# Performance work log

Hardware: AMD Instinct MI355X
Metric: run time of the kernel (lower is better)

## Reference

```python
import jax, jax.numpy as jnp
import numpy as np

HEADS = 8
DIM_HEAD = 64
SCALE = DIM_HEAD ** -0.5


def setup_inputs() -> dict:
    key = jax.random.key(0)
    ks = jax.random.split(key, 7)
    B, N, Dq = 2, 4096, 512
    M, Dc = 4096, 768
    inner = HEADS * DIM_HEAD  # 512
    x = jax.random.normal(ks[0], (B, N, Dq), dtype=jnp.float32)
    context = jax.random.normal(ks[1], (B, M, Dc), dtype=jnp.float32)
    # weights stored [in, out] (torch Linear weight transposed)
    Wq = jax.random.normal(ks[2], (Dq, inner), dtype=jnp.float32) * (Dq ** -0.5)
    Wk = jax.random.normal(ks[3], (Dc, inner), dtype=jnp.float32) * (Dc ** -0.5)
    Wv = jax.random.normal(ks[4], (Dc, inner), dtype=jnp.float32) * (Dc ** -0.5)
    Wo = jax.random.normal(ks[5], (inner, Dq), dtype=jnp.float32) * (inner ** -0.5)
    bo = jax.random.normal(ks[6], (Dq,), dtype=jnp.float32) * 0.01
    return {"x": x, "context": context, "Wq": Wq, "Wk": Wk, "Wv": Wv, "Wo": Wo, "bo": bo}


def reference(x, context, Wq, Wk, Wv, Wo, bo):
    B, N, _ = x.shape
    M = context.shape[1]
    h, d = HEADS, DIM_HEAD
    q = (x @ Wq).reshape(B, N, h, d)                      # b n h d
    k = ((context @ Wk) * SCALE).reshape(B, M, h, d)      # scale applied to k, as in source
    v = (context @ Wv).reshape(B, M, h, d)
    scores = jnp.einsum('bnhd,bmhd->bhnm', q, k)          # full QK^T
    attn = jax.nn.softmax(scores, axis=-1)
    out = jnp.einsum('bhnm,bmhd->bnhd', attn, v).reshape(B, N, h * d)
    return out @ Wo + bo  # dropout p=0.0 -> identity
```

## Files before the change

### kernel.cpp

```cpp
#include <hip/hip_runtime.h>

typedef unsigned short u16;
typedef __attribute__((ext_vector_type(4))) unsigned short u16x4;
typedef __attribute__((ext_vector_type(8))) unsigned short u16x8;
typedef __attribute__((ext_vector_type(8))) short s16x8;
typedef __attribute__((ext_vector_type(4))) float f32x4;
typedef __attribute__((ext_vector_type(16))) float f32x16;
typedef __attribute__((ext_vector_type(4))) unsigned int u32x4;

#define LOG2E 1.4426950408889634f

__device__ __forceinline__ u16 f2bf(float f) {
    return __builtin_bit_cast(unsigned short, static_cast<__bf16>(f));
}

__device__ __forceinline__ float bf2f(u16 v) {
    return __builtin_bit_cast(float, (unsigned)v << 16);
}

__device__ __forceinline__ float fexp2(float x) {
#if __has_builtin(__builtin_amdgcn_exp2f)
    return __builtin_amdgcn_exp2f(x);
#else
    return exp2f(x);
#endif
}

__device__ __forceinline__ s16x8 ld_frag(const u16* p) {
    return __builtin_bit_cast(s16x8, *reinterpret_cast<const u16x8*>(p));
}

__device__ __forceinline__ f32x4 mfma16(s16x8 a, s16x8 b, f32x4 c) {
    return __builtin_amdgcn_mfma_f32_16x16x32_bf16(a, b, c, 0, 0, 0);
}

__device__ __forceinline__ f32x16 mfma32(s16x8 a, s16x8 b, f32x16 c) {
    return __builtin_amdgcn_mfma_f32_32x32x16_bf16(a, b, c, 0, 0, 0);
}

__device__ __forceinline__ unsigned cvt_pk_bf16(float lo, float hi2) {
    unsigned r;
    asm("v_cvt_pk_bf16_f32 %0, %1, %2" : "=v"(r) : "v"(lo), "v"(hi2));
    return r;
}

__device__ __forceinline__ void plane32_swap(unsigned& x, unsigned& y) {
#if __has_builtin(__builtin_amdgcn_permlane32_swap)
    auto r = __builtin_amdgcn_permlane32_swap(x, y, false, false);
    x = r[0];
    y = r[1];
#else
    asm("v_permlane32_swap_b32 %0, %1" : "+v"(x), "+v"(y));
#endif
}

__device__ __forceinline__ void async16(const u16* g, u16* lds) {
    __builtin_amdgcn_global_load_lds(
        (__attribute__((address_space(1))) void*)const_cast<u16*>(g),
        (__attribute__((address_space(3))) void*)lds, 16, 0, 0);
}

__global__ __launch_bounds__(256) void cvt_fused_kernel(const float* __restrict__ x,
                                                        const float* __restrict__ ctx,
                                                        u16* __restrict__ xb,
                                                        u16* __restrict__ cb) {
    int i = blockIdx.x * 256 + threadIdx.x;
    const float* in;
    u16* out;
    int idx;
    if (i < 524288) {
        in = x; out = xb; idx = i;
    } else {
        in = ctx; out = cb; idx = i - 524288;
    }
    const f32x4* p = (const f32x4*)in + ((size_t)idx << 1);
    f32x4 a = p[0], c = p[1];
    u16x8 v;
    v[0] = f2bf(a[0]); v[1] = f2bf(a[1]); v[2] = f2bf(a[2]); v[3] = f2bf(a[3]);
    v[4] = f2bf(c[0]); v[5] = f2bf(c[1]); v[6] = f2bf(c[2]); v[7] = f2bf(c[3]);
    *((u16x8*)out + idx) = v;
}

__global__ __launch_bounds__(256) void wtrans4_kernel(
    const float* __restrict__ Wq, const float* __restrict__ Wk, const float* __restrict__ Wv,
    const float* __restrict__ Wo, u16* __restrict__ Wqt, u16* __restrict__ Wkt,
    u16* __restrict__ Wvt, u16* __restrict__ Wot) {
    __shared__ float t[32][33];
    const float* W;
    u16* Wt;
    int Kd;
    float scale;
    switch (blockIdx.z) {
        case 0: W = Wq; Wt = Wqt; Kd = 512; scale = 1.0f; break;
        case 1: W = Wk; Wt = Wkt; Kd = 768; scale = 0.125f * LOG2E; break;
        case 2: W = Wv; Wt = Wvt; Kd = 768; scale = 1.0f; break;
        default: W = Wo; Wt = Wot; Kd = 512; scale = 1.0f; break;
    }
    const int k0 = blockIdx.x << 5, n0 = blockIdx.y << 5;
    if (k0 >= Kd) return;
    const int tx = threadIdx.x, ty = threadIdx.y;
#pragma unroll
    for (int i = 0; i < 32; i += 8)
        t[ty + i][tx] = W[(size_t)(k0 + ty + i) * 512 + n0 + tx] * scale;
    __syncthreads();
#pragma unroll
    for (int i = 0; i < 32; i += 8)
        Wt[(size_t)(n0 + ty + i) * Kd + k0 + tx] = f2bf(t[tx][ty + i]);
}

template <int MODE>
__device__ __forceinline__ void gemm_body(u16* __restrict__ Ab, u16* __restrict__ Bb,
                                          const u16* __restrict__ A, const u16* __restrict__ Bt,
                                          void* __restrict__ Cv, const float* __restrict__ bias,
                                          int K) {
    const int tid = threadIdx.x;
    const int w = tid >> 6, l = tid & 63;
    const int lg = l >> 4, lq = l & 15;
    const int wm = w >> 1, wn = w & 1;
    const int bm = blockIdx.y, bn = blockIdx.x;
    const int KT = K >> 6;

    f32x4 acc[4][4];
#pragma unroll
    for (int i = 0; i < 4; i++)
#pragma unroll
        for (int j = 0; j < 4; j++) acc[i][j] = (f32x4){0.f, 0.f, 0.f, 0.f};

    const u16* Ag0 = A + (size_t)bm * 128 * K;
    const u16* Bg0 = Bt + (size_t)bn * 128 * K;
    const int srow = l >> 3, scol = (l & 7) << 3;

    auto stage = [&](int kt, int buf) {
#pragma unroll
        for (int i = 0; i < 4; i++) {
            const int c = (w << 2) + i;
            const int row = (c << 3) + srow;
            async16(Ag0 + (size_t)row * K + kt * 64 + scol, Ab + (buf << 13) + (c << 9));
            async16(Bg0 + (size_t)row * K + kt * 64 + scol, Bb + (buf << 13) + (c << 9));
        }
    };

    stage(0, 0);
    for (int kt = 0; kt < KT; ++kt) {
        __syncthreads();
        if (kt + 1 < KT) stage(kt + 1, (kt + 1) & 1);
        const u16* As = Ab + ((kt & 1) << 13);
        const u16* Bs = Bb + ((kt & 1) << 13);
#pragma unroll
        for (int s = 0; s < 2; s++) {
            s16x8 af[4], bfr[4];
#pragma unroll
            for (int mt = 0; mt < 4; mt++)
                af[mt] = ld_frag(As + ((wm << 6) + (mt << 4) + lq) * 64 + (s << 5) + (lg << 3));
#pragma unroll
            for (int nt = 0; nt < 4; nt++)
                bfr[nt] = ld_frag(Bs + ((wn << 6) + (nt << 4) + lq) * 64 + (s << 5) + (lg << 3));
#pragma unroll
            for (int mt = 0; mt < 4; mt++)
#pragma unroll
                for (int nt = 0; nt < 4; nt++)
                    acc[mt][nt] = mfma16(af[mt], bfr[nt], acc[mt][nt]);
        }
    }
    const int row0 = bm * 128 + (wm << 6);
    const int col0 = bn * 128 + (wn << 6);
    if constexpr (MODE == 0) {
        u16* C = (u16*)Cv;
#pragma unroll
        for (int mt = 0; mt < 4; mt++)
#pragma unroll
            for (int nt = 0; nt < 4; nt++)
#pragma unroll
                for (int r = 0; r < 4; r++)
                    C[(size_t)(row0 + (mt << 4) + (lg << 2) + r) * 512 + col0 + (nt << 4) + lq] =
                        f2bf(acc[mt][nt][r]);
    } else if constexpr (MODE == 3) {
        float* C = (float*)Cv;
        float bv[4];
#pragma unroll
        for (int nt = 0; nt < 4; nt++) bv[nt] = bias[col0 + (nt << 4) + lq];
#pragma unroll
        for (int mt = 0; mt < 4; mt++)
#pragma unroll
            for (int nt = 0; nt < 4; nt++)
#pragma unroll
                for (int r = 0; r < 4; r++)
                    C[(size_t)(row0 + (mt << 4) + (lg << 2) + r) * 512 + col0 + (nt << 4) + lq] =
                        acc[mt][nt][r] + bv[nt];
    } else {
        u16* C = (u16*)Cv;
#pragma unroll
        for (int mt = 0; mt < 4; mt++)
#pragma unroll
            for (int nt = 0; nt < 4; nt++)
#pragma unroll
                for (int r = 0; r < 4; r++) {
                    const int m = row0 + (mt << 4) + (lg << 2) + r;
                    const int feat = col0 + (nt << 4) + lq;
                    const int bh = ((m >> 12) << 3) + (feat >> 6);
                    const int d = feat & 63;
                    const int kv = m & 4095;
                    const int T = kv >> 5, kvl = kv & 31;
                    size_t off;
                    if constexpr (MODE == 1) {
                        const int lane = kvl + (((d >> 3) & 1) << 5);
                        off = ((size_t)(((bh << 7) + T) << 2) + (d >> 4)) * 512 + (lane << 3) +
                              (d & 7);
                    } else {
                        const int lane = (d & 31) + (((kvl >> 3) & 1) << 5);
                        const int fi = ((kvl >> 4) << 1) + (d >> 5);
                        off = ((size_t)(((bh << 7) + T) << 2) + fi) * 512 + (lane << 3) +
                              (kvl & 7);
                    }
                    C[off] = f2bf(acc[mt][nt][r]);
                }
    }
}

__global__ __launch_bounds__(256, 2) void proj_gemm_kernel(
    const u16* __restrict__ xb, const u16* __restrict__ cb, const u16* __restrict__ Wqt,
    const u16* __restrict__ Wkt, const u16* __restrict__ Wvt, u16* __restrict__ Qb,
    u16* __restrict__ Kp, u16* __restrict__ Vp) {
    __shared__ u16 Ab[2][8192];
    __shared__ u16 Bb[2][8192];
    const int z = blockIdx.z;
    if (z == 0)
        gemm_body<0>(&Ab[0][0], &Bb[0][0], xb, Wqt, Qb, nullptr, 512);
    else if (z == 1)
        gemm_body<1>(&Ab[0][0], &Bb[0][0], cb, Wkt, Kp, nullptr, 768);
    else
        gemm_body<2>(&Ab[0][0], &Bb[0][0], cb, Wvt, Vp, nullptr, 768);
}

__global__ __launch_bounds__(256, 2) void out_gemm_kernel(const u16* __restrict__ Ob,
                                                          const u16* __restrict__ Wot,
                                                          float* __restrict__ out,
                                                          const float* __restrict__ bias) {
    __shared__ u16 Ab[2][8192];
    __shared__ u16 Bb[2][8192];
    gemm_body<3>(&Ab[0][0], &Bb[0][0], Ob, Wot, out, bias, 512);
}

__global__ __launch_bounds__(256, 3) void attn_kernel(const u16* __restrict__ Qb,
                                                      const u16* __restrict__ Kp,
                                                      const u16* __restrict__ Vp,
                                                      u16* __restrict__ Opart,
                                                      float* __restrict__ Lpart) {
    __shared__ u16 Kl[2][2048];
    __shared__ u16 Vl[2][2048];
    const int tid = threadIdx.x;
    const int w = tid >> 6, l = tid & 63;
    const int lq = l & 31, hi = l >> 5;
    const int bid = blockIdx.x;
    const int swz = ((bid & 7) << 8) + (bid >> 3);
    const int bh = swz >> 7, qtg = (swz >> 2) & 31, kvseg = swz & 3;
    const int qt = (qtg << 2) + w;
    const int wid = (((bh << 7) + qt) << 2) + kvseg;
    const int b = bh >> 3, h = bh & 7;

    const u16* Qp = Qb + (size_t)(b * 4096 + (qt << 5) + lq) * 512 + (h << 6) + (hi << 3);
    s16x8 qf[4];
#pragma unroll
    for (int s = 0; s < 4; s++) qf[s] = ld_frag(Qp + (s << 4));

    const u16* Kg = Kp + ((size_t)(bh << 7) + (kvseg << 5)) * 2048;
    const u16* Vg = Vp + ((size_t)(bh << 7) + (kvseg << 5)) * 2048;
    const int gsrc = (w << 9) + (l << 3);
    const int ldst = w << 9;
    const int roff = l << 3;

    f32x16 oacc0 = {}, oacc1 = {};
    float rs = 0.f;

    async16(Kg + gsrc, &Kl[0][ldst]);
    async16(Vg + gsrc, &Vl[0][ldst]);

    for (int t = 0; t < 32; ++t) {
        const int buf = t & 1;
        __syncthreads();
        if (t + 1 < 32) {
            async16(Kg + (size_t)(t + 1) * 2048 + gsrc, &Kl[buf ^ 1][ldst]);
            async16(Vg + (size_t)(t + 1) * 2048 + gsrc, &Vl[buf ^ 1][ldst]);
        }
        const u16* Kb_ = Kl[buf];
        const u16* Vb_ = Vl[buf];

        s16x8 kf[4];
#pragma unroll
        for (int s = 0; s < 4; s++) kf[s] = ld_frag(Kb_ + (s << 9) + roff);
        f32x16 sacc = {};
        __builtin_amdgcn_s_setprio(1);
#pragma unroll
        for (int s = 0; s < 4; s++) sacc = mfma32(kf[s], qf[s], sacc);
        __builtin_amdgcn_s_setprio(0);

#pragma unroll
        for (int r = 0; r < 16; r++) sacc[r] = fexp2(sacc[r]);
        {
            float t0 = (sacc[0] + sacc[1]) + (sacc[2] + sacc[3]);
            float t1 = (sacc[4] + sacc[5]) + (sacc[6] + sacc[7]);
            float t2 = (sacc[8] + sacc[9]) + (sacc[10] + sacc[11]);
            float t3 = (sacc[12] + sacc[13]) + (sacc[14] + sacc[15]);
            rs += (t0 + t1) + (t2 + t3);
        }

        s16x8 aw[2];
#pragma unroll
        for (int sp = 0; sp < 2; sp++) {
            const int base2 = sp << 3;
            unsigned X1 = cvt_pk_bf16(sacc[base2 + 0], sacc[base2 + 1]);
            unsigned Y1 = cvt_pk_bf16(sacc[base2 + 4], sacc[base2 + 5]);
            unsigned X2 = cvt_pk_bf16(sacc[base2 + 2], sacc[base2 + 3]);
            unsigned Y2 = cvt_pk_bf16(sacc[base2 + 6], sacc[base2 + 7]);
            plane32_swap(X1, Y1);
            plane32_swap(X2, Y2);
            u32x4 wv;
            wv[0] = X1; wv[1] = X2; wv[2] = Y1; wv[3] = Y2;
            aw[sp] = __builtin_bit_cast(s16x8, wv);
        }

        s16x8 vf[4];
#pragma unroll
        for (int f = 0; f < 4; f++) vf[f] = ld_frag(Vb_ + (f << 9) + roff);
        __builtin_amdgcn_s_setprio(1);
#pragma unroll
        for (int sp = 0; sp < 2; sp++) {
            oacc0 = mfma32(aw[sp], vf[(sp << 1) + 0], oacc0);
            oacc1 = mfma32(aw[sp], vf[(sp << 1) + 1], oacc1);
        }
        __builtin_amdgcn_s_setprio(0);
    }

    u16* Ow = Opart + ((size_t)wid << 11);
#pragma unroll
    for (int r = 0; r < 16; r++) Ow[(r << 6) + l] = f2bf(oacc0[r]);
#pragma unroll
    for (int r = 0; r < 16; r++) Ow[((16 + r) << 6) + l] = f2bf(oacc1[r]);
    rs += __shfl_xor(rs, 32);
    if (l < 32) Lpart[(wid << 5) + l] = rs;
}

__global__ __launch_bounds__(256) void merge_kernel(const u16* __restrict__ Op,
                                                    const float* __restrict__ Lp,
                                                    u16* __restrict__ Ob) {
    const int g = blockIdx.x * 256 + threadIdx.x;
    const int slot = g >> 9;
    const int idx4 = (g & 511) << 2;
    const int dtr = idx4 >> 6;
    const int r = dtr & 15, dt = dtr >> 4;
    const int lane0 = idx4 & 63;
    const int q = (r & 3) + ((r >> 2) << 3) + ((lane0 >> 5) << 2);
    float lsum = 0.f;
#pragma unroll
    for (int p = 0; p < 4; p++) lsum += Lp[(slot << 7) + (p << 5) + q];
    const float ri = 1.f / lsum;
    float acc[4] = {0.f, 0.f, 0.f, 0.f};
#pragma unroll
    for (int p = 0; p < 4; p++) {
        const u16x4 a = *(const u16x4*)(Op + ((size_t)slot << 13) + (p << 11) + idx4);
#pragma unroll
        for (int j = 0; j < 4; j++) acc[j] += bf2f(a[j]);
    }
    u16x4 o;
#pragma unroll
    for (int j = 0; j < 4; j++) o[j] = f2bf(acc[j] * ri);
    const int bh = slot >> 7, qt = slot & 127;
    const int row = ((bh >> 3) << 12) + (qt << 5) + q;
    const int d = (lane0 & 31) + (dt << 5);
    *(u16x4*)(Ob + (size_t)row * 512 + ((bh & 7) << 6) + d) = o;
}

extern "C" void kernel_launch(void* const* d_in, const int* in_sizes, int n_in, void* d_out,
                              int out_size, void* d_ws, size_t ws_size, hipStream_t stream) {
    const float* x = (const float*)d_in[0];
    const float* ctx = (const float*)d_in[1];
    const float* Wq = (const float*)d_in[2];
    const float* Wk = (const float*)d_in[3];
    const float* Wv = (const float*)d_in[4];
    const float* Wo = (const float*)d_in[5];
    const float* bo = (const float*)d_in[6];
    float* out = (float*)d_out;

    char* ws = (char*)d_ws;
    u16* xb  = (u16*)(ws);
    u16* cb  = (u16*)(ws + 8388608);
    u16* Opart   = (u16*)(ws);
    float* Lpart = (float*)(ws + 33554432);
    u16* Qb  = (u16*)(ws + 34603008);
    u16* Ob  = (u16*)(ws + 34603008);
    u16* Kp  = (u16*)(ws + 42991616);
    u16* Vp  = (u16*)(ws + 51380224);
    u16* Wqt = (u16*)(ws + 59768832);
    u16* Wkt = (u16*)(ws + 60293120);
    u16* Wvt = (u16*)(ws + 61079552);
    u16* Wot = (u16*)(ws + 61865984);

    cvt_fused_kernel<<<dim3(5120), dim3(256), 0, stream>>>(x, ctx, xb, cb);
    wtrans4_kernel<<<dim3(24, 16, 4), dim3(32, 8), 0, stream>>>(Wq, Wk, Wv, Wo, Wqt, Wkt, Wvt,
                                                                Wot);
    proj_gemm_kernel<<<dim3(4, 64, 3), dim3(256), 0, stream>>>(xb, cb, Wqt, Wkt, Wvt, Qb, Kp, Vp);
    attn_kernel<<<dim3(2048), dim3(256), 0, stream>>>(Qb, Kp, Vp, Opart, Lpart);
    merge_kernel<<<dim3(4096), dim3(256), 0, stream>>>(Opart, Lpart, Ob);
    out_gemm_kernel<<<dim3(4, 64), dim3(256), 0, stream>>>(Ob, Wot, out, bo);
}
```

Measured before the change: 156.2 us.

## Fuse prep kernels, double attention KV tile per stage, widen merge vectors

Merges the fp32-to-bf16 conversion and weight transpose into a single prep launch, which removes one kernel launch. The attention loop now stages two 32-key sub-tiles per barrier (16 iterations instead of 32), halving sync count at the cost of double the LDS per block. The merge kernel handles 8 bf16 elements per thread with 128-bit loads and stores, halving its grid. The larger LDS footprint may reduce attention occupancy.

```diff
diff --git a/kernel.cpp b/kernel.cpp
--- a/kernel.cpp
+++ b/kernel.cpp
@@ -60,52 +60,56 @@
         (__attribute__((address_space(3))) void*)lds, 16, 0, 0);
 }
 
-__global__ __launch_bounds__(256) void cvt_fused_kernel(const float* __restrict__ x,
-                                                        const float* __restrict__ ctx,
-                                                        u16* __restrict__ xb,
-                                                        u16* __restrict__ cb) {
-    int i = blockIdx.x * 256 + threadIdx.x;
-    const float* in;
-    u16* out;
-    int idx;
-    if (i < 524288) {
-        in = x; out = xb; idx = i;
-    } else {
-        in = ctx; out = cb; idx = i - 524288;
-    }
-    const f32x4* p = (const f32x4*)in + ((size_t)idx << 1);
-    f32x4 a = p[0], c = p[1];
-    u16x8 v;
-    v[0] = f2bf(a[0]); v[1] = f2bf(a[1]); v[2] = f2bf(a[2]); v[3] = f2bf(a[3]);
-    v[4] = f2bf(c[0]); v[5] = f2bf(c[1]); v[6] = f2bf(c[2]); v[7] = f2bf(c[3]);
-    *((u16x8*)out + idx) = v;
-}
-
-__global__ __launch_bounds__(256) void wtrans4_kernel(
-    const float* __restrict__ Wq, const float* __restrict__ Wk, const float* __restrict__ Wv,
-    const float* __restrict__ Wo, u16* __restrict__ Wqt, u16* __restrict__ Wkt,
+__global__ __launch_bounds__(256) void prep_kernel(
+    const float* __restrict__ x, const float* __restrict__ ctx, const float* __restrict__ Wq,
+    const float* __restrict__ Wk, const float* __restrict__ Wv, const float* __restrict__ Wo,
+    u16* __restrict__ xb, u16* __restrict__ cb, u16* __restrict__ Wqt, u16* __restrict__ Wkt,
     u16* __restrict__ Wvt, u16* __restrict__ Wot) {
     __shared__ float t[32][33];
-    const float* W;
-    u16* Wt;
-    int Kd;
-    float scale;
-    switch (blockIdx.z) {
-        case 0: W = Wq; Wt = Wqt; Kd = 512; scale = 1.0f; break;
-        case 1: W = Wk; Wt = Wkt; Kd = 768; scale = 0.125f * LOG2E; break;
-        case 2: W = Wv; Wt = Wvt; Kd = 768; scale = 1.0f; break;
-        default: W = Wo; Wt = Wot; Kd = 512; scale = 1.0f; break;
+    const int bidx = blockIdx.x;
+    const int tid = threadIdx.x;
+    if (bidx < 5120) {
+        int i = bidx * 256 + tid;
+        const float* in;
+        u16* out;
+        int idx;
+        if (i < 524288) {
+            in = x; out = xb; idx = i;
+        } else {
+            in = ctx; out = cb; idx = i - 524288;
+        }
+        const f32x4* p = (const f32x4*)in + ((size_t)idx << 1);
+        f32x4 a = p[0], c = p[1];
+        u16x8 v;
+        v[0] = f2bf(a[0]); v[1] = f2bf(a[1]); v[2] = f2bf(a[2]); v[3] = f2bf(a[3]);
+        v[4] = f2bf(c[0]); v[5] = f2bf(c[1]); v[6] = f2bf(c[2]); v[7] = f2bf(c[3]);
+        *((u16x8*)out + idx) = v;
+    } else {
+        const int zb = bidx - 5120;
+        const int z = zb / 384;
+        const int rem = zb - z * 384;
+        const int kx = rem % 24, ny = rem / 24;
+        const float* W;
+        u16* Wt;
+        int Kd;
+        float scale;
+        switch (z) {
+            case 0: W = Wq; Wt = Wqt; Kd = 512; scale = 1.0f; break;
+            case 1: W = Wk; Wt = Wkt; Kd = 768; scale = 0.125f * LOG2E; break;
+            case 2: W = Wv; Wt = Wvt; Kd = 768; scale = 1.0f; break;
+            default: W = Wo; Wt = Wot; Kd = 512; scale = 1.0f; break;
+        }
+        const int k0 = kx << 5, n0 = ny << 5;
+        if (k0 >= Kd) return;
+        const int tx = tid & 31, ty = tid >> 5;
+#pragma unroll
+        for (int i = 0; i < 32; i += 8)
+            t[ty + i][tx] = W[(size_t)(k0 + ty + i) * 512 + n0 + tx] * scale;
+        __syncthreads();
+#pragma unroll
+        for (int i = 0; i < 32; i += 8)
+            Wt[(size_t)(n0 + ty + i) * Kd + k0 + tx] = f2bf(t[tx][ty + i]);
     }
-    const int k0 = blockIdx.x << 5, n0 = blockIdx.y << 5;
-    if (k0 >= Kd) return;
-    const int tx = threadIdx.x, ty = threadIdx.y;
-#pragma unroll
-    for (int i = 0; i < 32; i += 8)
-        t[ty + i][tx] = W[(size_t)(k0 + ty + i) * 512 + n0 + tx] * scale;
-    __syncthreads();
-#pragma unroll
-    for (int i = 0; i < 32; i += 8)
-        Wt[(size_t)(n0 + ty + i) * Kd + k0 + tx] = f2bf(t[tx][ty + i]);
 }
 
 template <int MODE>
@@ -246,8 +250,8 @@
                                                       const u16* __restrict__ Vp,
                                                       u16* __restrict__ Opart,
                                                       float* __restrict__ Lpart) {
-    __shared__ u16 Kl[2][2048];
-    __shared__ u16 Vl[2][2048];
+    __shared__ u16 Kl[2][4096];
+    __shared__ u16 Vl[2][4096];
     const int tid = threadIdx.x;
     const int w = tid >> 6, l = tid & 63;
     const int lq = l & 31, hi = l >> 5;
@@ -273,18 +277,11 @@
     float rs = 0.f;
 
     async16(Kg + gsrc, &Kl[0][ldst]);
+    async16(Kg + 2048 + gsrc, &Kl[0][2048 + ldst]);
     async16(Vg + gsrc, &Vl[0][ldst]);
-
-    for (int t = 0; t < 32; ++t) {
-        const int buf = t & 1;
-        __syncthreads();
-        if (t + 1 < 32) {
-            async16(Kg + (size_t)(t + 1) * 2048 + gsrc, &Kl[buf ^ 1][ldst]);
-            async16(Vg + (size_t)(t + 1) * 2048 + gsrc, &Vl[buf ^ 1][ldst]);
-        }
-        const u16* Kb_ = Kl[buf];
-        const u16* Vb_ = Vl[buf];
-
+    async16(Vg + 2048 + gsrc, &Vl[0][2048 + ldst]);
+
+    auto sub_body = [&](const u16* Kb_, const u16* Vb_) {
         s16x8 kf[4];
 #pragma unroll
         for (int s = 0; s < 4; s++) kf[s] = ld_frag(Kb_ + (s << 9) + roff);
@@ -329,6 +326,21 @@
             oacc1 = mfma32(aw[sp], vf[(sp << 1) + 1], oacc1);
         }
         __builtin_amdgcn_s_setprio(0);
+    };
+
+    for (int t = 0; t < 16; ++t) {
+        const int buf = t & 1;
+        __syncthreads();
+        if (t + 1 < 16) {
+            const size_t base = (size_t)(t + 1) * 4096;
+            const int nb = buf ^ 1;
+            async16(Kg + base + gsrc, &Kl[nb][ldst]);
+            async16(Kg + base + 2048 + gsrc, &Kl[nb][2048 + ldst]);
+            async16(Vg + base + gsrc, &Vl[nb][ldst]);
+            async16(Vg + base + 2048 + gsrc, &Vl[nb][2048 + ldst]);
+        }
+        sub_body(&Kl[buf][0], &Vl[buf][0]);
+        sub_body(&Kl[buf][2048], &Vl[buf][2048]);
     }
 
     u16* Ow = Opart + ((size_t)wid << 11);
@@ -344,30 +356,30 @@
                                                     const float* __restrict__ Lp,
                                                     u16* __restrict__ Ob) {
     const int g = blockIdx.x * 256 + threadIdx.x;
-    const int slot = g >> 9;
-    const int idx4 = (g & 511) << 2;
-    const int dtr = idx4 >> 6;
+    const int slot = g >> 8;
+    const int idx8 = (g & 255) << 3;
+    const int dtr = idx8 >> 6;
     const int r = dtr & 15, dt = dtr >> 4;
-    const int lane0 = idx4 & 63;
+    const int lane0 = idx8 & 63;
     const int q = (r & 3) + ((r >> 2) << 3) + ((lane0 >> 5) << 2);
     float lsum = 0.f;
 #pragma unroll
     for (int p = 0; p < 4; p++) lsum += Lp[(slot << 7) + (p << 5) + q];
     const float ri = 1.f / lsum;
-    float acc[4] = {0.f, 0.f, 0.f, 0.f};
+    float acc[8] = {0.f, 0.f, 0.f, 0.f, 0.f, 0.f, 0.f, 0.f};
 #pragma unroll
     for (int p = 0; p < 4; p++) {
-        const u16x4 a = *(const u16x4*)(Op + ((size_t)slot << 13) + (p << 11) + idx4);
-#pragma unroll
-        for (int j = 0; j < 4; j++) acc[j] += bf2f(a[j]);
+        const u16x8 a = *(const u16x8*)(Op + ((size_t)slot << 13) + (p << 11) + idx8);
+#pragma unroll
+        for (int j = 0; j < 8; j++) acc[j] += bf2f(a[j]);
     }
-    u16x4 o;
-#pragma unroll
-    for (int j = 0; j < 4; j++) o[j] = f2bf(acc[j] * ri);
+    u16x8 o;
+#pragma unroll
+    for (int j = 0; j < 8; j++) o[j] = f2bf(acc[j] * ri);
     const int bh = slot >> 7, qt = slot & 127;
     const int row = ((bh >> 3) << 12) + (qt << 5) + q;
     const int d = (lane0 & 31) + (dt << 5);
-    *(u16x4*)(Ob + (size_t)row * 512 + ((bh & 7) << 6) + d) = o;
+    *(u16x8*)(Ob + (size_t)row * 512 + ((bh & 7) << 6) + d) = o;
 }
 
 extern "C" void kernel_launch(void* const* d_in, const int* in_sizes, int n_in, void* d_out,
@@ -395,11 +407,10 @@
     u16* Wvt = (u16*)(ws + 61079552);
     u16* Wot = (u16*)(ws + 61865984);
 
-    cvt_fused_kernel<<<dim3(5120), dim3(256), 0, stream>>>(x, ctx, xb, cb);
-    wtrans4_kernel<<<dim3(24, 16, 4), dim3(32, 8), 0, stream>>>(Wq, Wk, Wv, Wo, Wqt, Wkt, Wvt,
-                                                                Wot);
+    prep_kernel<<<dim3(6656), dim3(256), 0, stream>>>(x, ctx, Wq, Wk, Wv, Wo, xb, cb, Wqt, Wkt,
+                                                      Wvt, Wot);
     proj_gemm_kernel<<<dim3(4, 64, 3), dim3(256), 0, stream>>>(xb, cb, Wqt, Wkt, Wvt, Qb, Kp, Vp);
     attn_kernel<<<dim3(2048), dim3(256), 0, stream>>>(Qb, Kp, Vp, Opart, Lpart);
-    merge_kernel<<<dim3(4096), dim3(256), 0, stream>>>(Opart, Lpart, Ob);
+    merge_kernel<<<dim3(2048), dim3(256), 0, stream>>>(Opart, Lpart, Ob);
     out_gemm_kernel<<<dim3(4, 64), dim3(256), 0, stream>>>(Ob, Wot, out, bo);
 }
```

Measured after the change: 155.2 us. Within noise of the previous version (-0.6%).
